# Kernel tuning notes

Measured on AMD Instinct MI355X. Metric: run time of the kernel, lower is better.

The kernel has to match this reference:

```python
import jax, jax.numpy as jnp
import numpy as np

N = 262144          # flattened node batch
IN_S, IN_V = 256, 32
OUT_S, OUT_V = 256, 32
H = max(IN_V, OUT_V)  # 32
EPS = 1e-4


def setup_inputs() -> dict:
    key = jax.random.key(0)
    ks = jax.random.split(key, 8)
    inv = lambda f: 1.0 / np.sqrt(f).astype(np.float32)
    return {
        "s": jax.random.normal(ks[0], (N, IN_S), jnp.float32),
        "V": jax.random.normal(ks[1], (N, IN_V, 3), jnp.float32),
        "W_h": jax.random.normal(ks[2], (H, IN_V), jnp.float32) * inv(IN_V),
        "W_mu": jax.random.normal(ks[3], (OUT_V, H), jnp.float32) * inv(H),
        "W_m_w": jax.random.normal(ks[4], (OUT_S, H + IN_S), jnp.float32) * inv(H + IN_S),
        "W_m_b": jax.random.normal(ks[5], (OUT_S,), jnp.float32) * 0.01,
        "W_g_w": jax.random.normal(ks[6], (OUT_V, OUT_S), jnp.float32) * inv(OUT_S),
        "W_g_b": jax.random.normal(ks[7], (OUT_V,), jnp.float32) * 0.01,
    }


def reference(s, V, W_h, W_mu, W_m_w, W_m_b, W_g_w, W_g_b):
    # V_h = W_h @ V : [N, H, 3]
    V_h = jnp.einsum('hv,nvc->nhc', W_h, V)
    # per-row L2 norm, clipped at eps : [N, H]
    s_h = jnp.maximum(jnp.linalg.norm(V_h, axis=-1), EPS)
    # Linear on concatenated scalars : [N, OUT_S]
    s_m = jnp.concatenate([s, s_h], axis=-1) @ W_m_w.T + W_m_b
    s_dash = jax.nn.relu(s_m)                      # sigma = relu
    # V_mu = W_mu @ V_h : [N, OUT_V, 3]
    V_mu = jnp.einsum('mh,nhc->nmc', W_mu, V_h)
    # vector gate: sigmoid(W_g(sigmoid(s_m)))  (sigma_plus = sigmoid)
    gate = jax.nn.sigmoid(jax.nn.sigmoid(s_m) @ W_g_w.T + W_g_b)  # [N, OUT_V]
    V_dash = gate[..., None] * V_mu
    return s_dash, V_dash
```

## Files before the change

### kernel.cpp

```cpp
#include <hip/hip_runtime.h>

#define NTOT 262144
#define BN   32
#define NT   256
#define SXS  296
#define VTS  36

typedef __attribute__((ext_vector_type(8))) short bf16x8;
typedef __attribute__((ext_vector_type(4))) float f32x4;

static __device__ __forceinline__ unsigned short f2b(float x) {
    union { float f; unsigned u; } c; c.f = x;
    unsigned r = c.u + 0x7FFFu + ((c.u >> 16) & 1u);
    return (unsigned short)(r >> 16);
}
static __device__ __forceinline__ float b2f(unsigned short h) {
    union { unsigned u; float f; } c; c.u = ((unsigned)h) << 16; return c.f;
}
static __device__ __forceinline__ bf16x8 cvt8(const float* p) {
    float4 x = *(const float4*)p, y = *(const float4*)(p + 4);
    bf16x8 r;
    r[0] = (short)f2b(x.x); r[1] = (short)f2b(x.y); r[2] = (short)f2b(x.z); r[3] = (short)f2b(x.w);
    r[4] = (short)f2b(y.x); r[5] = (short)f2b(y.y); r[6] = (short)f2b(y.z); r[7] = (short)f2b(y.w);
    return r;
}
static __device__ __forceinline__ void glds16(const unsigned short* g, void* l) {
    __builtin_amdgcn_global_load_lds(
        (const __attribute__((address_space(1))) void*)g,
        (__attribute__((address_space(3))) void*)l, 16, 0, 0);
}

__global__ void pack_w(const float* __restrict__ Wmw, const float* __restrict__ Wgw,
                       unsigned short* __restrict__ wp) {
    int t = blockIdx.x * 256 + threadIdx.x;
    if (t < 73728) {
        int o = t / 288, k = t % 288;
        int ks = k >> 5, kk = k & 31, ch = o >> 7, ol = o & 127;
        int kks = kk ^ (((ol >> 1) & 3) << 3);
        wp[(ks * 2 + ch) * 4096 + ol * 32 + kks] = f2b(Wmw[t]);
    } else if (t < 81920) {
        int j = t - 73728;
        int o = j >> 8, k = j & 255;
        wp[73728 + (k >> 5) * 1024 + o * 32 + (k & 31)] = f2b(Wgw[j]);
    }
}

template<int USE_WS>
__global__ __launch_bounds__(NT, 3)
void gvp_main(const float* __restrict__ s, const float* __restrict__ V,
              const float* __restrict__ Wh, const float* __restrict__ Wmu,
              const float* __restrict__ Wmw, const float* __restrict__ Wmb,
              const float* __restrict__ Wgw, const float* __restrict__ Wgb,
              const unsigned short* __restrict__ wpack,
              float* __restrict__ out)
{
    __shared__ __attribute__((aligned(16))) unsigned short sX[BN * SXS];
    __shared__ __attribute__((aligned(16))) unsigned short sWb[2 * 4096];
    __shared__ __attribute__((aligned(16))) unsigned short sVT[96 * VTS];

    const int t  = threadIdx.x;
    const int w  = t >> 6, l = t & 63;
    const int fr = l & 15, fq = l >> 4;
    const int n0 = blockIdx.x * BN;
    const int half = w & 1, oh = w >> 1;

    if (USE_WS) {
        #pragma unroll
        for (int c = 0; c < 2; ++c) {
            const unsigned short* src = wpack + c * 4096 + w * 1024 + l * 8;
            unsigned short* dst = sWb + c * 4096 + w * 1024;
            glds16(src, dst);
            glds16(src + 512, dst + 512);
        }
    }

    #pragma unroll
    for (int i = 0; i < 8; ++i) {
        int n = i * 4 + w;
        float4 x4 = *(const float4*)&s[(size_t)(n0 + n) * 256 + 4 * l];
        ushort4 h4; h4.x = f2b(x4.x); h4.y = f2b(x4.y); h4.z = f2b(x4.z); h4.w = f2b(x4.w);
        *(ushort4*)&sX[n * SXS + 4 * l] = h4;
    }
    {
        int n = t >> 3, vq = t & 7;
        const float* p = &V[(size_t)(n0 + n) * 96 + vq * 12];
        float4 q0 = *(const float4*)(p);
        float4 q1 = *(const float4*)(p + 4);
        float4 q2 = *(const float4*)(p + 8);
        ushort4 c0 = { f2b(q0.x), f2b(q0.w), f2b(q1.z), f2b(q2.y) };
        ushort4 c1 = { f2b(q0.y), f2b(q1.x), f2b(q1.w), f2b(q2.z) };
        ushort4 c2 = { f2b(q0.z), f2b(q1.y), f2b(q2.x), f2b(q2.w) };
        *(ushort4*)&sVT[(0 * 32 + n) * VTS + vq * 4] = c0;
        *(ushort4*)&sVT[(1 * 32 + n) * VTS + vq * 4] = c1;
        *(ushort4*)&sVT[(2 * 32 + n) * VTS + vq * 4] = c2;
    }
    if (!USE_WS) {
        #pragma unroll
        for (int c = 0; c < 2; ++c) {
            int ol = w * 32 + (l >> 1), kh = l & 1, x = (ol >> 1) & 3;
            const float* p = &Wmw[(c * 128 + ol) * 288 + kh * 16];
            unsigned short* dst = sWb + c * 4096;
            *(bf16x8*)&dst[ol * 32 + (((kh * 2 + 0) ^ x) << 3)] = cvt8(p);
            *(bf16x8*)&dst[ol * 32 + (((kh * 2 + 1) ^ x) << 3)] = cvt8(p + 8);
        }
    }
    __syncthreads();

    {
        bf16x8 bh = cvt8(&Wh[(oh * 16 + fr) * 32 + fq * 8]);
        f32x4 va0 = {0,0,0,0}, va1 = {0,0,0,0}, va2 = {0,0,0,0};
        bf16x8 a0 = *(const bf16x8*)&sVT[(0 * 32 + half * 16 + fr) * VTS + fq * 8];
        bf16x8 a1 = *(const bf16x8*)&sVT[(1 * 32 + half * 16 + fr) * VTS + fq * 8];
        bf16x8 a2 = *(const bf16x8*)&sVT[(2 * 32 + half * 16 + fr) * VTS + fq * 8];
        va0 = __builtin_amdgcn_mfma_f32_16x16x32_bf16(a0, bh, va0, 0, 0, 0);
        va1 = __builtin_amdgcn_mfma_f32_16x16x32_bf16(a1, bh, va1, 0, 0, 0);
        va2 = __builtin_amdgcn_mfma_f32_16x16x32_bf16(a2, bh, va2, 0, 0, 0);
        __syncthreads();
        #pragma unroll
        for (int r = 0; r < 4; ++r) {
            int nl = half * 16 + fq * 4 + r;
            int h  = oh * 16 + fr;
            sVT[(0 * 32 + nl) * VTS + h] = f2b(va0[r]);
            sVT[(1 * 32 + nl) * VTS + h] = f2b(va1[r]);
            sVT[(2 * 32 + nl) * VTS + h] = f2b(va2[r]);
            float nrm = sqrtf(fmaf(va0[r], va0[r], fmaf(va1[r], va1[r], va2[r] * va2[r])));
            sX[nl * SXS + 256 + h] = f2b(fmaxf(nrm, 1e-4f));
        }
    }
    __syncthreads();

    f32x4 acc[2][4];
    #pragma unroll
    for (int mt = 0; mt < 2; ++mt)
        #pragma unroll
        for (int j = 0; j < 4; ++j) acc[mt][j] = (f32x4){0.f, 0.f, 0.f, 0.f};

    const int ol0 = w * 32 + fr, ol1 = ol0 + 16;
    const int bo0 = ol0 * 32 + ((fq ^ ((ol0 >> 1) & 3)) << 3);
    const int bo1 = ol1 * 32 + ((fq ^ ((ol1 >> 1) & 3)) << 3);

    #pragma unroll
    for (int it = 0; it < 18; ++it) {
        if (it >= 2) {
            if (it <= 16) asm volatile("s_waitcnt vmcnt(2)" ::: "memory");
            else          asm volatile("s_waitcnt vmcnt(0)" ::: "memory");
            __builtin_amdgcn_sched_barrier(0);
        }
        const int ks = it >> 1;
        const unsigned short* bw = sWb + (it & 1) * 4096;
        bf16x8 a0 = *(const bf16x8*)&sX[fr * SXS + ks * 32 + fq * 8];
        bf16x8 a1 = *(const bf16x8*)&sX[(16 + fr) * SXS + ks * 32 + fq * 8];
        bf16x8 b0 = *(const bf16x8*)&bw[bo0];
        bf16x8 b1 = *(const bf16x8*)&bw[bo1];
        if (it < 16) {
            asm volatile("s_waitcnt lgkmcnt(0)" ::: "memory");
            __builtin_amdgcn_sched_barrier(0);
            if (USE_WS) {
                const unsigned short* src = wpack + (it + 2) * 4096 + w * 1024 + l * 8;
                unsigned short* dst = sWb + (it & 1) * 4096 + w * 1024;
                glds16(src, dst);
                glds16(src + 512, dst + 512);
            } else {
                int it2 = it + 2, ks2 = it2 >> 1, ch2 = it2 & 1;
                int ol = w * 32 + (l >> 1), kh = l & 1, x = (ol >> 1) & 3;
                const float* p = &Wmw[(ch2 * 128 + ol) * 288 + ks2 * 32 + kh * 16];
                unsigned short* dst = sWb + (it & 1) * 4096;
                *(bf16x8*)&dst[ol * 32 + (((kh * 2 + 0) ^ x) << 3)] = cvt8(p);
                *(bf16x8*)&dst[ol * 32 + (((kh * 2 + 1) ^ x) << 3)] = cvt8(p + 8);
            }
        }
        const int ji = (it & 1) * 2;
        acc[0][ji + 0] = __builtin_amdgcn_mfma_f32_16x16x32_bf16(a0, b0, acc[0][ji + 0], 0, 0, 0);
        acc[1][ji + 0] = __builtin_amdgcn_mfma_f32_16x16x32_bf16(a1, b0, acc[1][ji + 0], 0, 0, 0);
        acc[0][ji + 1] = __builtin_amdgcn_mfma_f32_16x16x32_bf16(a0, b1, acc[0][ji + 1], 0, 0, 0);
        acc[1][ji + 1] = __builtin_amdgcn_mfma_f32_16x16x32_bf16(a1, b1, acc[1][ji + 1], 0, 0, 0);
    }
    __syncthreads();

    float bias[4];
    #pragma unroll
    for (int ji = 0; ji < 4; ++ji)
        bias[ji] = Wmb[(ji >> 1) * 128 + w * 32 + (ji & 1) * 16 + fr];

    const int skw = ((fq & 1) << 4) | ((fq >> 1) << 3);
    float* sRel = (float*)sWb;
    #pragma unroll
    for (int mt = 0; mt < 2; ++mt) {
        #pragma unroll
        for (int r = 0; r < 4; ++r) {
            int row  = fq * 4 + r;
            int node = mt * 16 + row;
            #pragma unroll
            for (int ji = 0; ji < 4; ++ji) {
                int col = (ji >> 1) * 128 + w * 32 + (ji & 1) * 16 + fr;
                float m = acc[mt][ji][r] + bias[ji];
                sX[node * SXS + col] = f2b(1.f / (1.f + __expf(-m)));
                sRel[row * 256 + (col ^ skw)] = fmaxf(m, 0.f);
            }
        }
        __syncthreads();
        #pragma unroll
        for (int i = 0; i < 4; ++i) {
            int flat = i * NT + t;
            int row = flat >> 6, c4 = flat & 63;
            int sk2 = (((row >> 2) & 1) << 4) | (((row >> 3) & 1) << 3);
            float4 v4 = *(const float4*)&sRel[row * 256 + ((c4 * 4) ^ sk2)];
            *(float4*)&out[(size_t)(n0 + mt * 16 + row) * 256 + c4 * 4] = v4;
        }
        __syncthreads();
    }

    {
        const int gmt = w & 1, gnt = w >> 1;
        f32x4 g = (f32x4){0.f, 0.f, 0.f, 0.f};
        #pragma unroll
        for (int ks = 0; ks < 8; ++ks) {
            bf16x8 a = *(const bf16x8*)&sX[(gmt * 16 + fr) * SXS + ks * 32 + fq * 8];
            bf16x8 b;
            if (USE_WS) b = *(const bf16x8*)&wpack[73728 + ks * 1024 + (gnt * 16 + fr) * 32 + fq * 8];
            else        b = cvt8(&Wgw[(gnt * 16 + fr) * 256 + ks * 32 + fq * 8]);
            g = __builtin_amdgcn_mfma_f32_16x16x32_bf16(a, b, g, 0, 0, 0);
        }
        int mo = gnt * 16 + fr;
        float gb = Wgb[mo];
        #pragma unroll
        for (int r = 0; r < 4; ++r) {
            int node = gmt * 16 + fq * 4 + r;
            sX[node * SXS + 256 + mo] = f2b(1.f / (1.f + __expf(-(g[r] + gb))));
        }
    }
    __syncthreads();

    float* sc = (float*)sWb;
    {
        bf16x8 bm = cvt8(&Wmu[(oh * 16 + fr) * 32 + fq * 8]);
        f32x4 m0 = {0,0,0,0}, m1 = {0,0,0,0}, m2 = {0,0,0,0};
        bf16x8 a0 = *(const bf16x8*)&sVT[(0 * 32 + half * 16 + fr) * VTS + fq * 8];
        bf16x8 a1 = *(const bf16x8*)&sVT[(1 * 32 + half * 16 + fr) * VTS + fq * 8];
        bf16x8 a2 = *(const bf16x8*)&sVT[(2 * 32 + half * 16 + fr) * VTS + fq * 8];
        m0 = __builtin_amdgcn_mfma_f32_16x16x32_bf16(a0, bm, m0, 0, 0, 0);
        m1 = __builtin_amdgcn_mfma_f32_16x16x32_bf16(a1, bm, m1, 0, 0, 0);
        m2 = __builtin_amdgcn_mfma_f32_16x16x32_bf16(a2, bm, m2, 0, 0, 0);
        #pragma unroll
        for (int r = 0; r < 4; ++r) {
            int node = half * 16 + fq * 4 + r;
            int m    = oh * 16 + fr;
            float g  = b2f(sX[node * SXS + 256 + m]);
            sc[node * 96 + m * 3 + 0] = g * m0[r];
            sc[node * 96 + m * 3 + 1] = g * m1[r];
            sc[node * 96 + m * 3 + 2] = g * m2[r];
        }
    }
    __syncthreads();
    const size_t VBASE = (size_t)NTOT * 256;
    #pragma unroll
    for (int i = 0; i < 3; ++i) {
        int f = i * NT + t;
        *(float4*)&out[VBASE + (size_t)n0 * 96 + f * 4] = *(const float4*)&sc[f * 4];
    }
}

extern "C" void kernel_launch(void* const* d_in, const int* in_sizes, int n_in,
                              void* d_out, int out_size, void* d_ws, size_t ws_size,
                              hipStream_t stream) {
    const float* s   = (const float*)d_in[0];
    const float* V   = (const float*)d_in[1];
    const float* Wh  = (const float*)d_in[2];
    const float* Wmu = (const float*)d_in[3];
    const float* Wmw = (const float*)d_in[4];
    const float* Wmb = (const float*)d_in[5];
    const float* Wgw = (const float*)d_in[6];
    const float* Wgb = (const float*)d_in[7];
    float* out = (float*)d_out;

    dim3 grid(NTOT / BN);
    dim3 block(NT);

    if (ws_size >= 163840) {
        pack_w<<<320, 256, 0, stream>>>(Wmw, Wgw, (unsigned short*)d_ws);
        gvp_main<1><<<grid, block, 0, stream>>>(s, V, Wh, Wmu, Wmw, Wmb, Wgw, Wgb,
                                                (const unsigned short*)d_ws, out);
    } else {
        gvp_main<0><<<grid, block, 0, stream>>>(s, V, Wh, Wmu, Wmw, Wmb, Wgw, Wgb,
                                                nullptr, out);
    }
}
```

Measured before the change: 208.7 us.

## Shrink weight staging to triple-buffered 64-row chunks and keep gate in registers

```diff
diff --git a/kernel.cpp b/kernel.cpp
--- a/kernel.cpp
+++ b/kernel.cpp
@@ -13,9 +13,6 @@
     union { float f; unsigned u; } c; c.f = x;
     unsigned r = c.u + 0x7FFFu + ((c.u >> 16) & 1u);
     return (unsigned short)(r >> 16);
-}
-static __device__ __forceinline__ float b2f(unsigned short h) {
-    union { unsigned u; float f; } c; c.u = ((unsigned)h) << 16; return c.f;
 }
 static __device__ __forceinline__ bf16x8 cvt8(const float* p) {
     float4 x = *(const float4*)p, y = *(const float4*)(p + 4);
@@ -35,9 +32,9 @@
     int t = blockIdx.x * 256 + threadIdx.x;
     if (t < 73728) {
         int o = t / 288, k = t % 288;
-        int ks = k >> 5, kk = k & 31, ch = o >> 7, ol = o & 127;
+        int ks = k >> 5, kk = k & 31, q = o >> 6, ol = o & 63;
         int kks = kk ^ (((ol >> 1) & 3) << 3);
-        wp[(ks * 2 + ch) * 4096 + ol * 32 + kks] = f2b(Wmw[t]);
+        wp[(ks * 4 + q) * 2048 + ol * 32 + kks] = f2b(Wmw[t]);
     } else if (t < 81920) {
         int j = t - 73728;
         int o = j >> 8, k = j & 255;
@@ -55,7 +52,7 @@
               float* __restrict__ out)
 {
     __shared__ __attribute__((aligned(16))) unsigned short sX[BN * SXS];
-    __shared__ __attribute__((aligned(16))) unsigned short sWb[2 * 4096];
+    __shared__ __attribute__((aligned(16))) unsigned short sWb[3 * 2048];
     __shared__ __attribute__((aligned(16))) unsigned short sVT[96 * VTS];
 
     const int t  = threadIdx.x;
@@ -66,12 +63,8 @@
 
     if (USE_WS) {
         #pragma unroll
-        for (int c = 0; c < 2; ++c) {
-            const unsigned short* src = wpack + c * 4096 + w * 1024 + l * 8;
-            unsigned short* dst = sWb + c * 4096 + w * 1024;
-            glds16(src, dst);
-            glds16(src + 512, dst + 512);
-        }
+        for (int c = 0; c < 3; ++c)
+            glds16(wpack + c * 2048 + w * 512 + l * 8, &sWb[c * 2048 + w * 512]);
     }
 
     #pragma unroll
@@ -96,12 +89,11 @@
     }
     if (!USE_WS) {
         #pragma unroll
-        for (int c = 0; c < 2; ++c) {
-            int ol = w * 32 + (l >> 1), kh = l & 1, x = (ol >> 1) & 3;
-            const float* p = &Wmw[(c * 128 + ol) * 288 + kh * 16];
-            unsigned short* dst = sWb + c * 4096;
-            *(bf16x8*)&dst[ol * 32 + (((kh * 2 + 0) ^ x) << 3)] = cvt8(p);
-            *(bf16x8*)&dst[ol * 32 + (((kh * 2 + 1) ^ x) << 3)] = cvt8(p + 8);
+        for (int c = 0; c < 3; ++c) {
+            int ol = w * 16 + (l >> 2), kh = l & 3, x = (ol >> 1) & 3;
+            const float* p = &Wmw[(c * 64 + ol) * 288 + kh * 8];
+            sWb[c * 2048 + 0] = sWb[c * 2048 + 0];
+            *(bf16x8*)&sWb[c * 2048 + ol * 32 + ((kh ^ x) << 3)] = cvt8(p);
         }
     }
     __syncthreads();
@@ -135,67 +127,90 @@
         #pragma unroll
         for (int j = 0; j < 4; ++j) acc[mt][j] = (f32x4){0.f, 0.f, 0.f, 0.f};
 
-    const int ol0 = w * 32 + fr, ol1 = ol0 + 16;
+    const int ol0 = w * 16 + fr;
     const int bo0 = ol0 * 32 + ((fq ^ ((ol0 >> 1) & 3)) << 3);
-    const int bo1 = ol1 * 32 + ((fq ^ ((ol1 >> 1) & 3)) << 3);
-
-    #pragma unroll
-    for (int it = 0; it < 18; ++it) {
-        if (it >= 2) {
-            if (it <= 16) asm volatile("s_waitcnt vmcnt(2)" ::: "memory");
-            else          asm volatile("s_waitcnt vmcnt(0)" ::: "memory");
-            __builtin_amdgcn_sched_barrier(0);
-        }
-        const int ks = it >> 1;
-        const unsigned short* bw = sWb + (it & 1) * 4096;
+
+    #pragma unroll
+    for (int ks = 0; ks < 9; ++ks) {
         bf16x8 a0 = *(const bf16x8*)&sX[fr * SXS + ks * 32 + fq * 8];
         bf16x8 a1 = *(const bf16x8*)&sX[(16 + fr) * SXS + ks * 32 + fq * 8];
-        bf16x8 b0 = *(const bf16x8*)&bw[bo0];
-        bf16x8 b1 = *(const bf16x8*)&bw[bo1];
-        if (it < 16) {
-            asm volatile("s_waitcnt lgkmcnt(0)" ::: "memory");
-            __builtin_amdgcn_sched_barrier(0);
-            if (USE_WS) {
-                const unsigned short* src = wpack + (it + 2) * 4096 + w * 1024 + l * 8;
-                unsigned short* dst = sWb + (it & 1) * 4096 + w * 1024;
-                glds16(src, dst);
-                glds16(src + 512, dst + 512);
-            } else {
-                int it2 = it + 2, ks2 = it2 >> 1, ch2 = it2 & 1;
-                int ol = w * 32 + (l >> 1), kh = l & 1, x = (ol >> 1) & 3;
-                const float* p = &Wmw[(ch2 * 128 + ol) * 288 + ks2 * 32 + kh * 16];
-                unsigned short* dst = sWb + (it & 1) * 4096;
-                *(bf16x8*)&dst[ol * 32 + (((kh * 2 + 0) ^ x) << 3)] = cvt8(p);
-                *(bf16x8*)&dst[ol * 32 + (((kh * 2 + 1) ^ x) << 3)] = cvt8(p + 8);
-            }
-        }
-        const int ji = (it & 1) * 2;
-        acc[0][ji + 0] = __builtin_amdgcn_mfma_f32_16x16x32_bf16(a0, b0, acc[0][ji + 0], 0, 0, 0);
-        acc[1][ji + 0] = __builtin_amdgcn_mfma_f32_16x16x32_bf16(a1, b0, acc[1][ji + 0], 0, 0, 0);
-        acc[0][ji + 1] = __builtin_amdgcn_mfma_f32_16x16x32_bf16(a0, b1, acc[0][ji + 1], 0, 0, 0);
-        acc[1][ji + 1] = __builtin_amdgcn_mfma_f32_16x16x32_bf16(a1, b1, acc[1][ji + 1], 0, 0, 0);
+        #pragma unroll
+        for (int q = 0; q < 4; ++q) {
+            const int qi = ks * 4 + q;
+            if (qi >= 3) {
+                if (qi <= 33)      asm volatile("s_waitcnt vmcnt(2)" ::: "memory");
+                else if (qi == 34) asm volatile("s_waitcnt vmcnt(1)" ::: "memory");
+                else               asm volatile("s_waitcnt vmcnt(0)" ::: "memory");
+                __builtin_amdgcn_sched_barrier(0);
+            }
+            const unsigned short* bw = &sWb[(qi % 3) * 2048];
+            bf16x8 b0 = *(const bf16x8*)&bw[bo0];
+            if (qi <= 32) {
+                asm volatile("s_waitcnt lgkmcnt(0)" ::: "memory");
+                __builtin_amdgcn_sched_barrier(0);
+                if (USE_WS) {
+                    glds16(wpack + (qi + 3) * 2048 + w * 512 + l * 8,
+                           &sWb[(qi % 3) * 2048 + w * 512]);
+                } else {
+                    int qc = qi + 3, ks2 = qc >> 2, q2 = qc & 3;
+                    int ol = w * 16 + (l >> 2), kh = l & 3, x = (ol >> 1) & 3;
+                    const float* p = &Wmw[(q2 * 64 + ol) * 288 + ks2 * 32 + kh * 8];
+                    *(bf16x8*)&sWb[(qi % 3) * 2048 + ol * 32 + ((kh ^ x) << 3)] = cvt8(p);
+                }
+            }
+            acc[0][q] = __builtin_amdgcn_mfma_f32_16x16x32_bf16(a0, b0, acc[0][q], 0, 0, 0);
+            acc[1][q] = __builtin_amdgcn_mfma_f32_16x16x32_bf16(a1, b0, acc[1][q], 0, 0, 0);
+        }
     }
     __syncthreads();
 
     float bias[4];
     #pragma unroll
-    for (int ji = 0; ji < 4; ++ji)
-        bias[ji] = Wmb[(ji >> 1) * 128 + w * 32 + (ji & 1) * 16 + fr];
+    for (int q = 0; q < 4; ++q) bias[q] = Wmb[q * 64 + w * 16 + fr];
+
+    #pragma unroll
+    for (int mt = 0; mt < 2; ++mt)
+        #pragma unroll
+        for (int q = 0; q < 4; ++q) {
+            int col = q * 64 + w * 16 + fr;
+            #pragma unroll
+            for (int r = 0; r < 4; ++r) {
+                int node = mt * 16 + fq * 4 + r;
+                float m = acc[mt][q][r] + bias[q];
+                sX[node * SXS + col] = f2b(1.f / (1.f + __expf(-m)));
+            }
+        }
+    __syncthreads();
+
+    float gate[4];
+    {
+        f32x4 g = (f32x4){0.f, 0.f, 0.f, 0.f};
+        #pragma unroll
+        for (int ks = 0; ks < 8; ++ks) {
+            bf16x8 a = *(const bf16x8*)&sX[(half * 16 + fr) * SXS + ks * 32 + fq * 8];
+            bf16x8 b;
+            if (USE_WS) b = *(const bf16x8*)&wpack[73728 + ks * 1024 + (oh * 16 + fr) * 32 + fq * 8];
+            else        b = cvt8(&Wgw[(oh * 16 + fr) * 256 + ks * 32 + fq * 8]);
+            g = __builtin_amdgcn_mfma_f32_16x16x32_bf16(a, b, g, 0, 0, 0);
+        }
+        float gb = Wgb[oh * 16 + fr];
+        #pragma unroll
+        for (int r = 0; r < 4; ++r)
+            gate[r] = 1.f / (1.f + __expf(-(g[r] + gb)));
+    }
+    __syncthreads();
 
     const int skw = ((fq & 1) << 4) | ((fq >> 1) << 3);
-    float* sRel = (float*)sWb;
+    float* sRel = (float*)sX;
     #pragma unroll
     for (int mt = 0; mt < 2; ++mt) {
         #pragma unroll
         for (int r = 0; r < 4; ++r) {
-            int row  = fq * 4 + r;
-            int node = mt * 16 + row;
+            int row = fq * 4 + r;
             #pragma unroll
-            for (int ji = 0; ji < 4; ++ji) {
-                int col = (ji >> 1) * 128 + w * 32 + (ji & 1) * 16 + fr;
-                float m = acc[mt][ji][r] + bias[ji];
-                sX[node * SXS + col] = f2b(1.f / (1.f + __expf(-m)));
-                sRel[row * 256 + (col ^ skw)] = fmaxf(m, 0.f);
+            for (int q = 0; q < 4; ++q) {
+                int col = q * 64 + w * 16 + fr;
+                sRel[row * 256 + (col ^ skw)] = fmaxf(acc[mt][q][r] + bias[q], 0.f);
             }
         }
         __syncthreads();
@@ -210,28 +225,7 @@
         __syncthreads();
     }
 
-    {
-        const int gmt = w & 1, gnt = w >> 1;
-        f32x4 g = (f32x4){0.f, 0.f, 0.f, 0.f};
-        #pragma unroll
-        for (int ks = 0; ks < 8; ++ks) {
-            bf16x8 a = *(const bf16x8*)&sX[(gmt * 16 + fr) * SXS + ks * 32 + fq * 8];
-            bf16x8 b;
-            if (USE_WS) b = *(const bf16x8*)&wpack[73728 + ks * 1024 + (gnt * 16 + fr) * 32 + fq * 8];
-            else        b = cvt8(&Wgw[(gnt * 16 + fr) * 256 + ks * 32 + fq * 8]);
-            g = __builtin_amdgcn_mfma_f32_16x16x32_bf16(a, b, g, 0, 0, 0);
-        }
-        int mo = gnt * 16 + fr;
-        float gb = Wgb[mo];
-        #pragma unroll
-        for (int r = 0; r < 4; ++r) {
-            int node = gmt * 16 + fq * 4 + r;
-            sX[node * SXS + 256 + mo] = f2b(1.f / (1.f + __expf(-(g[r] + gb))));
-        }
-    }
-    __syncthreads();
-
-    float* sc = (float*)sWb;
+    float* sc = (float*)sX;
     {
         bf16x8 bm = cvt8(&Wmu[(oh * 16 + fr) * 32 + fq * 8]);
         f32x4 m0 = {0,0,0,0}, m1 = {0,0,0,0}, m2 = {0,0,0,0};
@@ -245,10 +239,9 @@
         for (int r = 0; r < 4; ++r) {
             int node = half * 16 + fq * 4 + r;
             int m    = oh * 16 + fr;
-            float g  = b2f(sX[node * SXS + 256 + m]);
-            sc[node * 96 + m * 3 + 0] = g * m0[r];
-            sc[node * 96 + m * 3 + 1] = g * m1[r];
-            sc[node * 96 + m * 3 + 2] = g * m2[r];
+            sc[node * 96 + m * 3 + 0] = gate[r] * m0[r];
+            sc[node * 96 + m * 3 + 1] = gate[r] * m1[r];
+            sc[node * 96 + m * 3 + 2] = gate[r] * m2[r];
         }
     }
     __syncthreads();
```

After: 216.7 us. 3.8% more time.
